# Kernel optimization log

Measured on AMD Instinct MI355X. Metric: run time of the kernel, lower is better.

Reference implementation:

```python
import jax, jax.numpy as jnp
import numpy as np

HEAD_SIZE = 64
N_EMBD = 128
B, T = 16, 2048


def setup_inputs() -> dict:
    key = jax.random.key(0)
    ks = jax.random.split(key, 7)
    s = 1.0 / np.sqrt(N_EMBD)
    return {
        "x": jax.random.normal(ks[0], (B, T, N_EMBD), dtype=jnp.float32),
        "Wk": jax.random.normal(ks[1], (N_EMBD, HEAD_SIZE), dtype=jnp.float32) * s,
        "bk": jax.random.normal(ks[2], (HEAD_SIZE,), dtype=jnp.float32) * s,
        "Wq": jax.random.normal(ks[3], (N_EMBD, HEAD_SIZE), dtype=jnp.float32) * s,
        "bq": jax.random.normal(ks[4], (HEAD_SIZE,), dtype=jnp.float32) * s,
        "Wv": jax.random.normal(ks[5], (N_EMBD, HEAD_SIZE), dtype=jnp.float32) * s,
        "bv": jax.random.normal(ks[6], (HEAD_SIZE,), dtype=jnp.float32) * s,
    }


def reference(x, Wk, bk, Wq, bq, Wv, bv):
    # x: [B, T, C]; single-head causal attention (dropout in eval mode = identity)
    Tdim = x.shape[1]
    k = x @ Wk + bk  # [B, T, H]
    q = x @ Wq + bq  # [B, T, H]
    v = x @ Wv + bv  # [B, T, H]
    scale = jnp.asarray(k.shape[-1], x.dtype) ** -0.5
    wei = jnp.einsum("bth,bsh->bts", q, k) * scale  # [B, T, T]
    causal = jnp.tril(jnp.ones((Tdim, Tdim), dtype=bool))
    wei = jnp.where(causal, wei, -jnp.inf)
    wei = jax.nn.softmax(wei, axis=-1)
    out = jnp.einsum("bts,bsh->bth", wei, v)  # [B, T, H]
    return out
```

## Files before the change

kernel.cpp:

```cpp
#include <hip/hip_runtime.h>
#include <hip/hip_bf16.h>
#include <math.h>

#define HS 64
#define NE 128
#define TSEQ 2048

typedef short s8v __attribute__((ext_vector_type(8)));
typedef float f4v __attribute__((ext_vector_type(4)));

__device__ __forceinline__ unsigned short f2bf(float f) {
    unsigned int u = __float_as_uint(f);
    u += 0x7FFFu + ((u >> 16) & 1u);
    return (unsigned short)(u >> 16);
}

__device__ __forceinline__ unsigned int pkbf(float a, float b) {
    union { __hip_bfloat162 h; unsigned int u; } cv;
    cv.h = __float22bfloat162_rn(make_float2(a, b));
    return cv.u;
}

__device__ __forceinline__ s8v mk_s8v(unsigned int a, unsigned int b,
                                      unsigned int c, unsigned int d) {
    union { unsigned int u[4]; s8v v; } cv;
    cv.u[0] = a; cv.u[1] = b; cv.u[2] = c; cv.u[3] = d;
    return cv.v;
}

__device__ __forceinline__ float fexp2(float x) {
    float r;
    asm("v_exp_f32 %0, %1" : "=v"(r) : "v"(x));
    return r;
}

__device__ __forceinline__ void glds16(const unsigned short* g, unsigned short* l) {
    __builtin_amdgcn_global_load_lds(
        (const __attribute__((address_space(1))) unsigned int*)g,
        (__attribute__((address_space(3))) unsigned int*)l,
        16, 0, 0);
}

__global__ __launch_bounds__(256) void wconv(
    const float* __restrict__ Wq, const float* __restrict__ Wk,
    const float* __restrict__ Wv, unsigned short* __restrict__ wt)
{
    const int o0 = (blockIdx.x * 256 + threadIdx.x) * 2;
    const int mat = o0 >> 13;
    const int n = (o0 >> 7) & 63;
    const int k = o0 & 127;
    const float* W = (mat == 0) ? Wq : (mat == 1) ? Wk : Wv;
    const float s = (mat == 0) ? 0.18033688f : 1.0f;
    unsigned int lo = f2bf(W[k * HS + n] * s);
    unsigned int hi = f2bf(W[(k + 1) * HS + n] * s);
    *(unsigned int*)(wt + o0) = lo | (hi << 16);
}

__global__ __launch_bounds__(256) void qkv(
    const float* __restrict__ x, const unsigned short* __restrict__ wt,
    const float* __restrict__ bq, const float* __restrict__ bk,
    const float* __restrict__ bv,
    unsigned short* __restrict__ qo, unsigned short* __restrict__ ko,
    unsigned short* __restrict__ vt)
{
    __shared__ __align__(16) unsigned short Ws[192 * 136];

    const int tid = threadIdx.x;
    const int w = tid >> 6;
    const int lane = tid & 63;
    const int quad = lane >> 4;
    const int li = lane & 15;
    const size_t blk0 = (size_t)blockIdx.x * 64;
    const size_t row0w = blk0 + (size_t)w * 16;

#pragma unroll
    for (int p = 0; p < 12; ++p) {
        const int idx = p * 256 + tid;
        const int n = idx >> 4;
        const int c = idx & 15;
        s8v d = *(const s8v*)(wt + idx * 8);
        *(s8v*)&Ws[n * 136 + c * 8] = d;
    }

    s8v a[4];
    const float* xr = x + (row0w + li) * NE + quad * 8;
#pragma unroll
    for (int ks = 0; ks < 4; ++ks) {
        float4 f0 = *(const float4*)(xr + ks * 32);
        float4 f1 = *(const float4*)(xr + ks * 32 + 4);
        a[ks] = mk_s8v(pkbf(f0.x, f0.y), pkbf(f0.z, f0.w),
                       pkbf(f1.x, f1.y), pkbf(f1.z, f1.w));
    }

    __syncthreads();

    f4v acc[12];
#pragma unroll
    for (int nt = 0; nt < 12; ++nt) acc[nt] = (f4v){0.f, 0.f, 0.f, 0.f};

#pragma unroll
    for (int nt = 0; nt < 12; ++nt) {
        const unsigned short* wr = &Ws[(nt * 16 + li) * 136 + quad * 8];
#pragma unroll
        for (int ks = 0; ks < 4; ++ks) {
            s8v bfr = *(const s8v*)(wr + ks * 32);
            acc[nt] = __builtin_amdgcn_mfma_f32_16x16x32_bf16(a[ks], bfr, acc[nt], 0, 0, 0);
        }
    }

    const size_t bidx = row0w >> 11;
    const size_t trow0 = row0w & 2047;
#pragma unroll
    for (int nt = 0; nt < 4; ++nt) {
        const float bias = bv[nt * 16 + li];
        unsigned int lo = pkbf(acc[nt + 8][0] + bias, acc[nt + 8][1] + bias);
        unsigned int hi = pkbf(acc[nt + 8][2] + bias, acc[nt + 8][3] + bias);
        *(uint2*)(vt + (bidx * HS + nt * 16 + li) * TSEQ + trow0 + quad * 4) =
            make_uint2(lo, hi);
    }

    __syncthreads();

    float* Qt = (float*)Ws;
    float* Kt = Qt + 64 * 68;
    const float sq = 0.18033688f;
    const int lrow0 = w * 16 + quad * 4;
#pragma unroll
    for (int nt = 0; nt < 4; ++nt) {
        const int col = nt * 16 + li;
        const float bq_ = bq[col] * sq;
        const float bk_ = bk[col];
#pragma unroll
        for (int r = 0; r < 4; ++r) {
            Qt[(lrow0 + r) * 68 + col] = acc[nt][r] + bq_;
            Kt[(lrow0 + r) * 68 + col] = acc[nt + 4][r] + bk_;
        }
    }

    __syncthreads();

    const int row = tid >> 2;
    const int seg = tid & 3;
    {
        const float* src = &Qt[row * 68 + seg * 16];
        float4 f0 = *(const float4*)src;
        float4 f1 = *(const float4*)(src + 4);
        float4 f2 = *(const float4*)(src + 8);
        float4 f3 = *(const float4*)(src + 12);
        s8v d0 = mk_s8v(pkbf(f0.x, f0.y), pkbf(f0.z, f0.w), pkbf(f1.x, f1.y), pkbf(f1.z, f1.w));
        s8v d1 = mk_s8v(pkbf(f2.x, f2.y), pkbf(f2.z, f2.w), pkbf(f3.x, f3.y), pkbf(f3.z, f3.w));
        unsigned short* dst = qo + (blk0 + row) * HS + seg * 16;
        *(s8v*)dst = d0;
        *(s8v*)(dst + 8) = d1;
    }
    {
        const float* src = &Kt[row * 68 + seg * 16];
        float4 f0 = *(const float4*)src;
        float4 f1 = *(const float4*)(src + 4);
        float4 f2 = *(const float4*)(src + 8);
        float4 f3 = *(const float4*)(src + 12);
        s8v d0 = mk_s8v(pkbf(f0.x, f0.y), pkbf(f0.z, f0.w), pkbf(f1.x, f1.y), pkbf(f1.z, f1.w));
        s8v d1 = mk_s8v(pkbf(f2.x, f2.y), pkbf(f2.z, f2.w), pkbf(f3.x, f3.y), pkbf(f3.z, f3.w));
        unsigned short* dst = ko + (blk0 + row) * HS + seg * 16;
        *(s8v*)dst = d0;
        *(s8v*)(dst + 8) = d1;
    }
}

__global__ __launch_bounds__(256) void attn_main(
    const unsigned short* __restrict__ qb,
    const unsigned short* __restrict__ kb,
    const unsigned short* __restrict__ vtb,
    float* __restrict__ out, float* __restrict__ pbuf, float* __restrict__ lsbuf)
{
    __shared__ unsigned short Ks[2][64 * 64];
    __shared__ unsigned short Vs[2][64 * 64];
    __shared__ __align__(16) unsigned short Ps[4][1024];

    const int tid = threadIdx.x;
    const int w = tid >> 6;
    const int lane = tid & 63;
    const int quad = lane >> 4;
    const int li = lane & 15;

    const int id = blockIdx.x;
    const int b = id / 80;
    const int u = 79 - (id - b * 80);
    int qt, c, nc;
    if (u < 8)       { qt = u;                 c = 0;            nc = 1; }
    else if (u < 24) { qt = 8 + ((u - 8) >> 1);  c = (u - 8) & 1;  nc = 2; }
    else if (u < 48) { qt = 16 + (u - 24) / 3;   c = (u - 24) % 3; nc = 3; }
    else             { qt = 24 + ((u - 48) >> 2); c = (u - 48) & 3; nc = 4; }
    const int tb = c * 8;
    const int te_ = tb + 8;
    const int te = (te_ < qt + 1) ? te_ : (qt + 1);

    const size_t base = (size_t)b * TSEQ;
    const int t0 = qt << 6;
    const int qrow = t0 + w * 16 + li;

    const unsigned short* qrp = qb + (base + qrow) * HS + quad * 8;
    s8v qf0 = *(const s8v*)qrp;
    s8v qf1 = *(const s8v*)(qrp + 32);

    const int rA = w * 8 + (lane >> 3);
    const int csw = (lane & 7) ^ (rA & 7);
    const unsigned short* kgA = kb + (base + rA) * HS + csw * 8;
    const unsigned short* kgB = kgA + 32 * HS;
    const unsigned short* vgA = vtb + ((size_t)b * HS + rA) * TSEQ + csw * 8;
    const unsigned short* vgB = vgA + 32 * TSEQ;
    const int ldsA = w * 512 + lane * 8;
    const int ldsB = 2048 + w * 512 + lane * 8;

    glds16(kgA + (size_t)tb * 4096, &Ks[0][ldsA]);
    glds16(kgB + (size_t)tb * 4096, &Ks[0][ldsB]);
    glds16(vgA + (size_t)tb * 64,   &Vs[0][ldsA]);
    glds16(vgB + (size_t)tb * 64,   &Vs[0][ldsB]);

    f4v c_o[4];
#pragma unroll
    for (int f = 0; f < 4; ++f) c_o[f] = (f4v){0.f, 0.f, 0.f, 0.f};
    float lsum = 0.f;

    char* pbse = (char*)&Ps[w][0];
    const int swz0 = (quad ^ (li & 7)) * 8;
    const int swz1 = ((4 + quad) ^ (li & 7)) * 8;

    __syncthreads();

    for (int tl = tb; tl < te; ++tl) {
        const int bi = (tl - tb) & 1;
        if (tl + 1 < te) {
            const int nb = bi ^ 1;
            glds16(kgA + (size_t)(tl + 1) * 4096, &Ks[nb][ldsA]);
            glds16(kgB + (size_t)(tl + 1) * 4096, &Ks[nb][ldsB]);
            glds16(vgA + (size_t)(tl + 1) * 64,   &Vs[nb][ldsA]);
            glds16(vgB + (size_t)(tl + 1) * 64,   &Vs[nb][ldsB]);
        }
        const unsigned short* Kc = &Ks[bi][0];
        const unsigned short* Vc = &Vs[bi][0];
        const bool diag = (tl == qt);

        float pr[4][4];
        float rs = 0.f;
#pragma unroll
        for (int kt = 0; kt < 4; ++kt) {
            const unsigned short* krow = Kc + (kt * 16 + li) * 64;
            s8v k0 = *(const s8v*)(krow + swz0);
            s8v k1 = *(const s8v*)(krow + swz1);
            f4v cst = (f4v){0.f, 0.f, 0.f, 0.f};
            cst = __builtin_amdgcn_mfma_f32_16x16x32_bf16(k0, qf0, cst, 0, 0, 0);
            cst = __builtin_amdgcn_mfma_f32_16x16x32_bf16(k1, qf1, cst, 0, 0, 0);
            if (diag) {
                const int key0 = (tl << 6) + kt * 16 + quad * 4;
#pragma unroll
                for (int rr = 0; rr < 4; ++rr)
                    if (key0 + rr > qrow) cst[rr] = -INFINITY;
            }
#pragma unroll
            for (int rr = 0; rr < 4; ++rr) {
                pr[kt][rr] = fexp2(cst[rr]);
                rs += pr[kt][rr];
            }
        }
        lsum += rs;

#pragma unroll
        for (int kt = 0; kt < 4; ++kt) {
            *(uint2*)(pbse + (kt * 2 + (quad >> 1)) * 256 + li * 16 + (quad & 1) * 8) =
                make_uint2(pkbf(pr[kt][0], pr[kt][1]), pkbf(pr[kt][2], pr[kt][3]));
        }
        s8v pf0 = *(const s8v*)(pbse + lane * 16);
        s8v pf1 = *(const s8v*)(pbse + 1024 + lane * 16);

#pragma unroll
        for (int f = 0; f < 4; ++f) {
            const unsigned short* vrow = Vc + (f * 16 + li) * 64;
            s8v v0 = *(const s8v*)(vrow + swz0);
            s8v v1 = *(const s8v*)(vrow + swz1);
            c_o[f] = __builtin_amdgcn_mfma_f32_16x16x32_bf16(v0, pf0, c_o[f], 0, 0, 0);
            c_o[f] = __builtin_amdgcn_mfma_f32_16x16x32_bf16(v1, pf1, c_o[f], 0, 0, 0);
        }

        __syncthreads();
    }

    lsum += __shfl_xor(lsum, 16);
    lsum += __shfl_xor(lsum, 32);

    if (nc == 1) {
        const float inv = 1.0f / lsum;
        float* orow = out + (base + qrow) * HS + quad * 4;
#pragma unroll
        for (int f = 0; f < 4; ++f) {
            f4v res = c_o[f];
            res[0] *= inv; res[1] *= inv; res[2] *= inv; res[3] *= inv;
            *(f4v*)(orow + f * 16) = res;
        }
    } else {
        const int local = (qt < 16) ? (qt - 8) * 2 + c
                        : (qt < 24) ? 16 + (qt - 16) * 3 + c
                                    : 40 + (qt - 24) * 4 + c;
        const int pidx = b * 72 + local;
        float* pc = pbuf + (size_t)pidx * 4096 + (w * 16 + li) * 64;
#pragma unroll
        for (int f = 0; f < 4; ++f)
            *(f4v*)(pc + f * 16 + quad * 4) = c_o[f];
        if (quad == 0)
            lsbuf[(size_t)pidx * 64 + w * 16 + li] = lsum;
    }
}

__global__ __launch_bounds__(256) void attn_reduce(
    const float* __restrict__ pbuf, const float* __restrict__ lsbuf,
    float* __restrict__ out)
{
    const int g = blockIdx.x;
    const int b = g / 24;
    const int r = g - b * 24;
    int qt, lbase, nc;
    if (r < 8)       { qt = 8 + r;        lbase = 2 * r;            nc = 2; }
    else if (r < 16) { qt = 16 + (r - 8); lbase = 16 + 3 * (r - 8); nc = 3; }
    else             { qt = 24 + (r - 16); lbase = 40 + 4 * (r - 16); nc = 4; }
    const int pidx0 = b * 72 + lbase;

    const int tid = threadIdx.x;
    const int row = tid >> 2;
    const int seg = tid & 3;

    float4 acc[4];
#pragma unroll
    for (int j = 0; j < 4; ++j) acc[j] = make_float4(0.f, 0.f, 0.f, 0.f);
    float ls = 0.f;

    for (int cc = 0; cc < nc; ++cc) {
        const float* pc = pbuf + (size_t)(pidx0 + cc) * 4096 + row * 64 + seg * 16;
#pragma unroll
        for (int j = 0; j < 4; ++j) {
            float4 v = *(const float4*)(pc + j * 4);
            acc[j].x += v.x; acc[j].y += v.y; acc[j].z += v.z; acc[j].w += v.w;
        }
        ls += lsbuf[(size_t)(pidx0 + cc) * 64 + row];
    }
    const float inv = 1.0f / ls;
    float* orow = out + ((size_t)b * TSEQ + (qt << 6) + row) * HS + seg * 16;
#pragma unroll
    for (int j = 0; j < 4; ++j) {
        *(float4*)(orow + j * 4) = make_float4(acc[j].x * inv, acc[j].y * inv,
                                               acc[j].z * inv, acc[j].w * inv);
    }
}

extern "C" void kernel_launch(void* const* d_in, const int* in_sizes, int n_in,
                              void* d_out, int out_size, void* d_ws, size_t ws_size,
                              hipStream_t stream) {
    const float* x  = (const float*)d_in[0];
    const float* Wk = (const float*)d_in[1];
    const float* bk = (const float*)d_in[2];
    const float* Wq = (const float*)d_in[3];
    const float* bq = (const float*)d_in[4];
    const float* Wv = (const float*)d_in[5];
    const float* bv = (const float*)d_in[6];
    float* outp = (float*)d_out;

    const size_t elems = (size_t)16 * TSEQ * HS;
    unsigned short* qbuf = (unsigned short*)d_ws;
    unsigned short* kbuf = qbuf + elems;
    unsigned short* vbuf = kbuf + elems;
    unsigned short* wtb  = vbuf + elems;
    float* pbuf  = (float*)(wtb + 32768);
    float* lsbuf = pbuf + (size_t)1152 * 4096;

    wconv<<<48, 256, 0, stream>>>(Wq, Wk, Wv, wtb);
    qkv<<<512, 256, 0, stream>>>(x, wtb, bq, bk, bv, qbuf, kbuf, vbuf);
    attn_main<<<1280, 256, 0, stream>>>(qbuf, kbuf, vbuf, outp, pbuf, lsbuf);
    attn_reduce<<<384, 256, 0, stream>>>(pbuf, lsbuf, outp);
}
```

Baseline: 114.4 us.

## Swap MFMA operands in QKV projection to write outputs directly without LDS staging

The QKV projection kernel now computes the transposed product (weights as A operand, x as B operand), so each lane holds consecutive head dimensions for one token. It can then add bias and store Q and K as bf16 straight to global memory, with no shared-memory transpose and no barriers. Weights are read from global memory instead of being staged in LDS, and the launch moves to one 64-thread wave per 16 tokens. The trade-off is that every wave rereads the whole weight matrix from cache, and the V-transpose stores become scattered 2-byte writes.

```diff
diff --git a/kernel.cpp b/kernel.cpp
--- a/kernel.cpp
+++ b/kernel.cpp
@@ -56,114 +56,70 @@
     *(unsigned int*)(wt + o0) = lo | (hi << 16);
 }
 
-__global__ __launch_bounds__(256) void qkv(
+__global__ __launch_bounds__(64) void qkv(
     const float* __restrict__ x, const unsigned short* __restrict__ wt,
     const float* __restrict__ bq, const float* __restrict__ bk,
     const float* __restrict__ bv,
     unsigned short* __restrict__ qo, unsigned short* __restrict__ ko,
     unsigned short* __restrict__ vt)
 {
-    __shared__ __align__(16) unsigned short Ws[192 * 136];
-
     const int tid = threadIdx.x;
-    const int w = tid >> 6;
-    const int lane = tid & 63;
-    const int quad = lane >> 4;
-    const int li = lane & 15;
-    const size_t blk0 = (size_t)blockIdx.x * 64;
-    const size_t row0w = blk0 + (size_t)w * 16;
-
-#pragma unroll
-    for (int p = 0; p < 12; ++p) {
-        const int idx = p * 256 + tid;
-        const int n = idx >> 4;
-        const int c = idx & 15;
-        s8v d = *(const s8v*)(wt + idx * 8);
-        *(s8v*)&Ws[n * 136 + c * 8] = d;
-    }
-
-    s8v a[4];
-    const float* xr = x + (row0w + li) * NE + quad * 8;
+    const int quad = tid >> 4;
+    const int li = tid & 15;
+    const size_t t0 = (size_t)blockIdx.x * 16;
+    const size_t t = t0 + li;
+
+    s8v xb[4];
+    const float* xr = x + t * NE + quad * 8;
 #pragma unroll
     for (int ks = 0; ks < 4; ++ks) {
         float4 f0 = *(const float4*)(xr + ks * 32);
         float4 f1 = *(const float4*)(xr + ks * 32 + 4);
-        a[ks] = mk_s8v(pkbf(f0.x, f0.y), pkbf(f0.z, f0.w),
-                       pkbf(f1.x, f1.y), pkbf(f1.z, f1.w));
-    }
-
-    __syncthreads();
+        xb[ks] = mk_s8v(pkbf(f0.x, f0.y), pkbf(f0.z, f0.w),
+                        pkbf(f1.x, f1.y), pkbf(f1.z, f1.w));
+    }
 
     f4v acc[12];
 #pragma unroll
-    for (int nt = 0; nt < 12; ++nt) acc[nt] = (f4v){0.f, 0.f, 0.f, 0.f};
-
-#pragma unroll
-    for (int nt = 0; nt < 12; ++nt) {
-        const unsigned short* wr = &Ws[(nt * 16 + li) * 136 + quad * 8];
+    for (int mt = 0; mt < 12; ++mt) acc[mt] = (f4v){0.f, 0.f, 0.f, 0.f};
+
+#pragma unroll
+    for (int mt = 0; mt < 12; ++mt) {
+        const unsigned short* wr = wt + (mt * 16 + li) * NE + quad * 8;
 #pragma unroll
         for (int ks = 0; ks < 4; ++ks) {
-            s8v bfr = *(const s8v*)(wr + ks * 32);
-            acc[nt] = __builtin_amdgcn_mfma_f32_16x16x32_bf16(a[ks], bfr, acc[nt], 0, 0, 0);
-        }
-    }
-
-    const size_t bidx = row0w >> 11;
-    const size_t trow0 = row0w & 2047;
-#pragma unroll
-    for (int nt = 0; nt < 4; ++nt) {
-        const float bias = bv[nt * 16 + li];
-        unsigned int lo = pkbf(acc[nt + 8][0] + bias, acc[nt + 8][1] + bias);
-        unsigned int hi = pkbf(acc[nt + 8][2] + bias, acc[nt + 8][3] + bias);
-        *(uint2*)(vt + (bidx * HS + nt * 16 + li) * TSEQ + trow0 + quad * 4) =
-            make_uint2(lo, hi);
-    }
-
-    __syncthreads();
-
-    float* Qt = (float*)Ws;
-    float* Kt = Qt + 64 * 68;
+            s8v af = *(const s8v*)(wr + ks * 32);
+            acc[mt] = __builtin_amdgcn_mfma_f32_16x16x32_bf16(af, xb[ks], acc[mt], 0, 0, 0);
+        }
+    }
+
+    const int d0 = quad * 4;
     const float sq = 0.18033688f;
-    const int lrow0 = w * 16 + quad * 4;
-#pragma unroll
-    for (int nt = 0; nt < 4; ++nt) {
-        const int col = nt * 16 + li;
-        const float bq_ = bq[col] * sq;
-        const float bk_ = bk[col];
+
+#pragma unroll
+    for (int mt = 0; mt < 4; ++mt) {
+        float4 bb = *(const float4*)(bq + mt * 16 + d0);
+        *(ushort4*)(qo + t * HS + mt * 16 + d0) = (ushort4){
+            f2bf(acc[mt][0] + bb.x * sq), f2bf(acc[mt][1] + bb.y * sq),
+            f2bf(acc[mt][2] + bb.z * sq), f2bf(acc[mt][3] + bb.w * sq)};
+    }
+#pragma unroll
+    for (int mt = 0; mt < 4; ++mt) {
+        float4 bb = *(const float4*)(bk + mt * 16 + d0);
+        *(ushort4*)(ko + t * HS + mt * 16 + d0) = (ushort4){
+            f2bf(acc[mt + 4][0] + bb.x), f2bf(acc[mt + 4][1] + bb.y),
+            f2bf(acc[mt + 4][2] + bb.z), f2bf(acc[mt + 4][3] + bb.w)};
+    }
+    const size_t bidx = t0 >> 11;
+    const size_t trow = t & 2047;
+#pragma unroll
+    for (int mt = 0; mt < 4; ++mt) {
+        float4 bb = *(const float4*)(bv + mt * 16 + d0);
 #pragma unroll
         for (int r = 0; r < 4; ++r) {
-            Qt[(lrow0 + r) * 68 + col] = acc[nt][r] + bq_;
-            Kt[(lrow0 + r) * 68 + col] = acc[nt + 4][r] + bk_;
-        }
-    }
-
-    __syncthreads();
-
-    const int row = tid >> 2;
-    const int seg = tid & 3;
-    {
-        const float* src = &Qt[row * 68 + seg * 16];
-        float4 f0 = *(const float4*)src;
-        float4 f1 = *(const float4*)(src + 4);
-        float4 f2 = *(const float4*)(src + 8);
-        float4 f3 = *(const float4*)(src + 12);
-        s8v d0 = mk_s8v(pkbf(f0.x, f0.y), pkbf(f0.z, f0.w), pkbf(f1.x, f1.y), pkbf(f1.z, f1.w));
-        s8v d1 = mk_s8v(pkbf(f2.x, f2.y), pkbf(f2.z, f2.w), pkbf(f3.x, f3.y), pkbf(f3.z, f3.w));
-        unsigned short* dst = qo + (blk0 + row) * HS + seg * 16;
-        *(s8v*)dst = d0;
-        *(s8v*)(dst + 8) = d1;
-    }
-    {
-        const float* src = &Kt[row * 68 + seg * 16];
-        float4 f0 = *(const float4*)src;
-        float4 f1 = *(const float4*)(src + 4);
-        float4 f2 = *(const float4*)(src + 8);
-        float4 f3 = *(const float4*)(src + 12);
-        s8v d0 = mk_s8v(pkbf(f0.x, f0.y), pkbf(f0.z, f0.w), pkbf(f1.x, f1.y), pkbf(f1.z, f1.w));
-        s8v d1 = mk_s8v(pkbf(f2.x, f2.y), pkbf(f2.z, f2.w), pkbf(f3.x, f3.y), pkbf(f3.z, f3.w));
-        unsigned short* dst = ko + (blk0 + row) * HS + seg * 16;
-        *(s8v*)dst = d0;
-        *(s8v*)(dst + 8) = d1;
+            vt[(bidx * HS + mt * 16 + d0 + r) * TSEQ + trow] =
+                f2bf(acc[mt + 8][r] + (&bb.x)[r]);
+        }
     }
 }
 
@@ -372,7 +328,7 @@
     float* lsbuf = pbuf + (size_t)1152 * 4096;
 
     wconv<<<48, 256, 0, stream>>>(Wq, Wk, Wv, wtb);
-    qkv<<<512, 256, 0, stream>>>(x, wtb, bq, bk, bv, qbuf, kbuf, vbuf);
+    qkv<<<2048, 64, 0, stream>>>(x, wtb, bq, bk, bv, qbuf, kbuf, vbuf);
     attn_main<<<1280, 256, 0, stream>>>(qbuf, kbuf, vbuf, outp, pbuf, lsbuf);
     attn_reduce<<<384, 256, 0, stream>>>(pbuf, lsbuf, outp);
 }
```

Result: slower. 124.0 us (+8.4%).
